# Optimization experiments

Measured on AMD Instinct MI355X. Metric: run time of the kernel, lower is better.

## Reference

```python
import jax, jax.numpy as jnp
import numpy as np

N_NODES = 100000
N_EDGES = 400000
DIM = 3
HID = 32


def _glorot(key, shape):
    fan_in, fan_out = shape[0], shape[1]
    lim = np.sqrt(6.0 / (fan_in + fan_out))
    return jax.random.uniform(key, shape, jnp.float32, -lim, lim)


def setup_inputs() -> dict:
    key = jax.random.key(0)
    ks = jax.random.split(key, 12)
    x = jax.random.normal(ks[0], (N_NODES, DIM), jnp.float32)
    edge_index = jax.random.randint(ks[1], (2, N_EDGES), 0, N_NODES, jnp.int64)
    edge_attr = jax.random.normal(ks[2], (N_EDGES, DIM), jnp.float32)
    params = {
        # conv1: NNConv(3 -> 32), edge nn = Linear(3, 3*32)
        'Wn1': _glorot(ks[3], (DIM, DIM * HID)), 'bn1': jnp.zeros((DIM * HID,), jnp.float32),
        'root1': _glorot(ks[4], (DIM, HID)), 'b1': jnp.zeros((HID,), jnp.float32),
        # conv2: NNConv(32 -> 32), edge nn = Linear(3, 32*32)
        'Wn2': _glorot(ks[5], (DIM, HID * HID)), 'bn2': jnp.zeros((HID * HID,), jnp.float32),
        'root2': _glorot(ks[6], (HID, HID)), 'b2': jnp.zeros((HID,), jnp.float32),
        # fc layers
        'Wf1': _glorot(ks[7], (HID, HID)), 'bf1': jnp.zeros((HID,), jnp.float32),
        'Wf2': _glorot(ks[8], (HID, 1)), 'bf2': jnp.zeros((1,), jnp.float32),
    }
    return {'x': x, 'edge_index': edge_index, 'edge_attr': edge_attr, **params}


def _nnconv(x, src, dst, edge_attr, Wn, bn, root, b, in_c, out_c):
    # per-edge weight matrix from edge MLP: [E, in_c, out_c]
    We = (edge_attr @ Wn + bn).reshape(-1, in_c, out_c)
    # gather source features, per-edge matmul, scatter-add to destinations
    msg = jnp.einsum('ei,eio->eo', x[src], We)  # [E, out_c]
    agg = jax.ops.segment_sum(msg, dst, num_segments=x.shape[0])  # [N, out_c]
    return agg + x @ root + b


def reference(x, edge_index, edge_attr, Wn1, bn1, root1, b1, Wn2, bn2, root2, b2, Wf1, bf1, Wf2, bf2):
    src, dst = edge_index[0], edge_index[1]
    h = jax.nn.relu(_nnconv(x, src, dst, edge_attr, Wn1, bn1, root1, b1, DIM, HID))
    h = jax.nn.relu(_nnconv(h, src, dst, edge_attr, Wn2, bn2, root2, b2, HID, HID))
    h = jax.nn.relu(h @ Wf1 + bf1)
    return h @ Wf2 + bf2  # [N, 1]
```

## Files before the change

kernel.cpp:

```cpp
#include <hip/hip_runtime.h>
#include <hip/hip_fp16.h>

#define N_NODES 100000
#define N_EDGES 400000
#define SCAN_BLOCKS ((N_NODES + 255) / 256)

__global__ __launch_bounds__(256) void zero_kernel(int4* __restrict__ deg4) {
    int i = blockIdx.x * 256 + threadIdx.x;
    if (i < N_NODES / 4) deg4[i] = make_int4(0, 0, 0, 0);
}

__global__ __launch_bounds__(256) void hist_kernel(const int* __restrict__ ei,
                                                   int* __restrict__ deg) {
    int e = blockIdx.x * 256 + threadIdx.x;
    if (e < N_EDGES) atomicAdd(&deg[ei[N_EDGES + e]], 1);
}

__global__ __launch_bounds__(256) void scanA_kernel(const int* __restrict__ deg,
                                                    int* __restrict__ rowptr,
                                                    int* __restrict__ psum) {
    __shared__ int sm[256];
    int i = blockIdx.x * 256 + threadIdx.x;
    int v = (i < N_NODES) ? deg[i] : 0;
    sm[threadIdx.x] = v;
    __syncthreads();
    #pragma unroll
    for (int off = 1; off < 256; off <<= 1) {
        int t = (threadIdx.x >= off) ? sm[threadIdx.x - off] : 0;
        __syncthreads();
        sm[threadIdx.x] += t;
        __syncthreads();
    }
    if (i < N_NODES) rowptr[i] = sm[threadIdx.x] - v;
    if (threadIdx.x == 255) psum[blockIdx.x] = sm[255];
}

__global__ __launch_bounds__(256) void scanBC_kernel(const int* __restrict__ psum,
                                                     int* __restrict__ rowptr,
                                                     int* __restrict__ cursor) {
    __shared__ int sm[8];
    int bid = blockIdx.x, tid = threadIdx.x;
    int acc = 0;
    for (int t = tid; t < bid; t += 256) acc += psum[t];
    #pragma unroll
    for (int off = 32; off; off >>= 1) acc += __shfl_down(acc, off, 64);
    if ((tid & 63) == 0) sm[tid >> 6] = acc;
    __syncthreads();
    int base = sm[0] + sm[1] + sm[2] + sm[3];
    int i = bid * 256 + tid;
    if (i < N_NODES) {
        int r = rowptr[i] + base;
        rowptr[i] = r;
        cursor[i] = r;
    }
    if (i == 0) rowptr[N_NODES] = N_EDGES;
}

__global__ __launch_bounds__(256) void scatter_kernel(const int* __restrict__ ei,
                                                      const float* __restrict__ ea,
                                                      const float* __restrict__ x,
                                                      int* __restrict__ cursor,
                                                      float4* __restrict__ edataA,
                                                      float4* __restrict__ edataB) {
    int e = blockIdx.x * 256 + threadIdx.x;
    if (e >= N_EDGES) return;
    int s = ei[e], d = ei[N_EDGES + e];
    int pos = atomicAdd(&cursor[d], 1);
    edataA[pos] = make_float4(ea[e*3], ea[e*3+1], ea[e*3+2], __int_as_float(s));
    edataB[pos] = make_float4(x[s*3], x[s*3+1], x[s*3+2], 0.f);
}

__global__ __launch_bounds__(256) void conv1_kernel(const int* __restrict__ rowptr,
                                                    const float4* __restrict__ edataA,
                                                    const float4* __restrict__ edataB,
                                                    const float* __restrict__ x,
                                                    const float* __restrict__ Wn1,
                                                    const float* __restrict__ bn1,
                                                    const float* __restrict__ root1,
                                                    const float* __restrict__ b1,
                                                    float* __restrict__ h1) {
    int gid = blockIdx.x * 256 + threadIdx.x;
    int n = gid >> 5, o = gid & 31;
    if (n >= N_NODES) return;
    float W[3][3], bb[3];
    #pragma unroll
    for (int d2 = 0; d2 < 3; ++d2)
        #pragma unroll
        for (int d = 0; d < 3; ++d) W[d2][d] = Wn1[d2*96 + d*32 + o];
    #pragma unroll
    for (int d = 0; d < 3; ++d) bb[d] = bn1[d*32 + o];

    int j0 = rowptr[n], j1 = rowptr[n + 1];
    float acc0 = 0.f, acc1 = 0.f;
    int j = j0;
    for (; j + 2 <= j1; j += 2) {
        float4 eA0 = edataA[j],   eB0 = edataB[j];
        float4 eA1 = edataA[j+1], eB1 = edataB[j+1];
        float wd0 = fmaf(eA0.x, W[0][0], fmaf(eA0.y, W[1][0], fmaf(eA0.z, W[2][0], bb[0])));
        float wd1 = fmaf(eA0.x, W[0][1], fmaf(eA0.y, W[1][1], fmaf(eA0.z, W[2][1], bb[1])));
        float wd2 = fmaf(eA0.x, W[0][2], fmaf(eA0.y, W[1][2], fmaf(eA0.z, W[2][2], bb[2])));
        acc0 += fmaf(eB0.x, wd0, fmaf(eB0.y, wd1, eB0.z * wd2));
        float ud0 = fmaf(eA1.x, W[0][0], fmaf(eA1.y, W[1][0], fmaf(eA1.z, W[2][0], bb[0])));
        float ud1 = fmaf(eA1.x, W[0][1], fmaf(eA1.y, W[1][1], fmaf(eA1.z, W[2][1], bb[1])));
        float ud2 = fmaf(eA1.x, W[0][2], fmaf(eA1.y, W[1][2], fmaf(eA1.z, W[2][2], bb[2])));
        acc1 += fmaf(eB1.x, ud0, fmaf(eB1.y, ud1, eB1.z * ud2));
    }
    if (j < j1) {
        float4 eA0 = edataA[j], eB0 = edataB[j];
        float wd0 = fmaf(eA0.x, W[0][0], fmaf(eA0.y, W[1][0], fmaf(eA0.z, W[2][0], bb[0])));
        float wd1 = fmaf(eA0.x, W[0][1], fmaf(eA0.y, W[1][1], fmaf(eA0.z, W[2][1], bb[1])));
        float wd2 = fmaf(eA0.x, W[0][2], fmaf(eA0.y, W[1][2], fmaf(eA0.z, W[2][2], bb[2])));
        acc0 += fmaf(eB0.x, wd0, fmaf(eB0.y, wd1, eB0.z * wd2));
    }
    float v = acc0 + acc1 + b1[o];
    v = fmaf(x[n*3],   root1[o],      v);
    v = fmaf(x[n*3+1], root1[32 + o], v);
    v = fmaf(x[n*3+2], root1[64 + o], v);
    h1[(size_t)n*32 + o] = fmaxf(v, 0.f);
}

__global__ __launch_bounds__(256) void prep2_kernel(const float* __restrict__ h1,
                                                    const float* __restrict__ Wn2,
                                                    const float* __restrict__ bn2,
                                                    uint2* __restrict__ G2h) {
    int o = threadIdx.x & 31;
    float w0[32], w1[32], w2[32], w3[32];
    #pragma unroll
    for (int i = 0; i < 32; ++i) {
        w0[i] = Wn2[         i*32 + o];
        w1[i] = Wn2[1024 +   i*32 + o];
        w2[i] = Wn2[2048 +   i*32 + o];
        w3[i] = bn2[         i*32 + o];
    }
    int g = (blockIdx.x * 256 + threadIdx.x) >> 5;
    int gstep = (gridDim.x * 256) >> 5;
    for (int n = g; n < N_NODES; n += gstep) {
        const float* __restrict__ hr = h1 + (size_t)n * 32;
        float g0 = 0.f, g1 = 0.f, g2 = 0.f, g3 = 0.f;
        #pragma unroll
        for (int i = 0; i < 32; ++i) {
            float hi = hr[i];
            g0 = fmaf(hi, w0[i], g0);
            g1 = fmaf(hi, w1[i], g1);
            g2 = fmaf(hi, w2[i], g2);
            g3 = fmaf(hi, w3[i], g3);
        }
        __half2 ab = __floats2half2_rn(g0, g1);
        __half2 cd = __floats2half2_rn(g2, g3);
        uint2 p;
        p.x = *(const unsigned int*)&ab;
        p.y = *(const unsigned int*)&cd;
        G2h[(size_t)n*32 + o] = p;
    }
}

__global__ __launch_bounds__(256) void conv2_kernel(const int* __restrict__ rowptr,
                                                    const float4* __restrict__ edataA,
                                                    const uint2* __restrict__ G2h,
                                                    float* __restrict__ h2pre) {
    int gid = blockIdx.x * 256 + threadIdx.x;
    int n = gid >> 5, o = gid & 31;
    if (n >= N_NODES) return;
    int j0 = rowptr[n], j1 = rowptr[n + 1];
    float a0 = 0.f, a1 = 0.f;
    int j = j0;
    for (; j + 2 <= j1; j += 2) {
        float4 e0 = edataA[j], e1 = edataA[j+1];
        uint2 p0 = G2h[(size_t)__float_as_int(e0.w)*32 + o];
        uint2 p1 = G2h[(size_t)__float_as_int(e1.w)*32 + o];
        float2 f0a = __half22float2(*(const __half2*)&p0.x);
        float2 f0b = __half22float2(*(const __half2*)&p0.y);
        float2 f1a = __half22float2(*(const __half2*)&p1.x);
        float2 f1b = __half22float2(*(const __half2*)&p1.y);
        a0 += fmaf(e0.x, f0a.x, fmaf(e0.y, f0a.y, fmaf(e0.z, f0b.x, f0b.y)));
        a1 += fmaf(e1.x, f1a.x, fmaf(e1.y, f1a.y, fmaf(e1.z, f1b.x, f1b.y)));
    }
    if (j < j1) {
        float4 e0 = edataA[j];
        uint2 p0 = G2h[(size_t)__float_as_int(e0.w)*32 + o];
        float2 f0a = __half22float2(*(const __half2*)&p0.x);
        float2 f0b = __half22float2(*(const __half2*)&p0.y);
        a0 += fmaf(e0.x, f0a.x, fmaf(e0.y, f0a.y, fmaf(e0.z, f0b.x, f0b.y)));
    }
    h2pre[(size_t)n*32 + o] = a0 + a1;
}

__global__ __launch_bounds__(256) void node2_kernel(const float* __restrict__ h2pre,
                                                    const float* __restrict__ h1,
                                                    const float* __restrict__ root2,
                                                    const float* __restrict__ b2,
                                                    const float* __restrict__ Wf1,
                                                    const float* __restrict__ bf1,
                                                    const float* __restrict__ Wf2,
                                                    const float* __restrict__ bf2,
                                                    float* __restrict__ out) {
    int n = blockIdx.x * 256 + threadIdx.x;
    if (n >= N_NODES) return;
    float hr[32];
    const float4* hv = (const float4*)(h1 + (size_t)n * 32);
    #pragma unroll
    for (int j4 = 0; j4 < 8; ++j4) {
        float4 t = hv[j4];
        hr[j4*4+0] = t.x; hr[j4*4+1] = t.y; hr[j4*4+2] = t.z; hr[j4*4+3] = t.w;
    }
    const float4* av = (const float4*)(h2pre + (size_t)n * 32);
    float h2[32];
    #pragma unroll
    for (int j4 = 0; j4 < 8; ++j4) {
        float4 a = av[j4];
        #pragma unroll
        for (int k = 0; k < 4; ++k) {
            int j = j4*4 + k;
            float acc = (&a.x)[k] + b2[j];
            #pragma unroll
            for (int i = 0; i < 32; ++i)
                acc = fmaf(hr[i], root2[i*32 + j], acc);
            h2[j] = fmaxf(acc, 0.f);
        }
    }
    float acc2 = bf2[0];
    #pragma unroll
    for (int j = 0; j < 32; ++j) {
        float a = bf1[j];
        #pragma unroll
        for (int i = 0; i < 32; ++i) a = fmaf(h2[i], Wf1[i*32 + j], a);
        acc2 = fmaf(fmaxf(a, 0.f), Wf2[j], acc2);
    }
    out[n] = acc2;
}

extern "C" void kernel_launch(void* const* d_in, const int* in_sizes, int n_in,
                              void* d_out, int out_size, void* d_ws, size_t ws_size,
                              hipStream_t stream) {
    const float* x     = (const float*)d_in[0];
    const int*   ei    = (const int*)  d_in[1];
    const float* ea    = (const float*)d_in[2];
    const float* Wn1   = (const float*)d_in[3];
    const float* bn1   = (const float*)d_in[4];
    const float* root1 = (const float*)d_in[5];
    const float* b1    = (const float*)d_in[6];
    const float* Wn2   = (const float*)d_in[7];
    const float* bn2   = (const float*)d_in[8];
    const float* root2 = (const float*)d_in[9];
    const float* b2    = (const float*)d_in[10];
    const float* Wf1   = (const float*)d_in[11];
    const float* bf1   = (const float*)d_in[12];
    const float* Wf2   = (const float*)d_in[13];
    const float* bf2   = (const float*)d_in[14];
    float* out = (float*)d_out;

    float*  h1     = (float*)d_ws;
    float*  h2pre  = h1 + (size_t)N_NODES*32;
    uint2*  G2h    = (uint2*)(h2pre + (size_t)N_NODES*32);
    float4* edataA = (float4*)(G2h + (size_t)N_NODES*32);
    float4* edataB = edataA + N_EDGES;
    int*    deg    = (int*)(edataB + N_EDGES);
    int*    rowptr = deg + N_NODES;
    int*    cursor = rowptr + N_NODES + 1;
    int*    psum   = cursor + N_NODES;

    int eb   = (N_EDGES + 255) / 256;
    int nb   = (N_NODES + 255) / 256;
    int nb32 = (N_NODES * 32 + 255) / 256;
    int zb   = (N_NODES / 4 + 255) / 256;

    zero_kernel   <<<zb, 256, 0, stream>>>((int4*)deg);
    hist_kernel   <<<eb, 256, 0, stream>>>(ei, deg);
    scanA_kernel  <<<SCAN_BLOCKS, 256, 0, stream>>>(deg, rowptr, psum);
    scanBC_kernel <<<SCAN_BLOCKS, 256, 0, stream>>>(psum, rowptr, cursor);
    scatter_kernel<<<eb, 256, 0, stream>>>(ei, ea, x, cursor, edataA, edataB);
    conv1_kernel  <<<nb32, 256, 0, stream>>>(rowptr, edataA, edataB, x, Wn1, bn1, root1, b1, h1);
    prep2_kernel  <<<1536, 256, 0, stream>>>(h1, Wn2, bn2, G2h);
    conv2_kernel  <<<nb32, 256, 0, stream>>>(rowptr, edataA, G2h, h2pre);
    node2_kernel  <<<nb, 256, 0, stream>>>(h2pre, h1, root2, b2, Wf1, bf1, Wf2, bf2, out);
}
```

Before: 150.1 us.

## Fuse CSR build into cooperative kernel, gather x in conv1, precompute root2 in prep2

Replaces the five CSR-construction launches with a single cooperative kernel that uses grid-wide syncs between the zero, histogram, scan and scatter phases. It drops the edataB buffer, so conv1 now gathers source features from x by index instead. prep2 is reorganised to use 64-lane waves that also compute h1·root2, stored as fp16, so node2 no longer runs a 32x32 matmul per node. The trade-offs are grid-sync overhead, more random gathers in conv1, and extra fp16 rounding on the root term. node2 also contains leftover redundant loads and conversions.

Result: slower. 327.9 us (+118.4%).

```diff
diff --git a/kernel.cpp b/kernel.cpp
--- a/kernel.cpp
+++ b/kernel.cpp
@@ -1,78 +1,78 @@
 #include <hip/hip_runtime.h>
 #include <hip/hip_fp16.h>
+#include <hip/hip_cooperative_groups.h>
 
 #define N_NODES 100000
 #define N_EDGES 400000
-#define SCAN_BLOCKS ((N_NODES + 255) / 256)
-
-__global__ __launch_bounds__(256) void zero_kernel(int4* __restrict__ deg4) {
-    int i = blockIdx.x * 256 + threadIdx.x;
-    if (i < N_NODES / 4) deg4[i] = make_int4(0, 0, 0, 0);
-}
-
-__global__ __launch_bounds__(256) void hist_kernel(const int* __restrict__ ei,
-                                                   int* __restrict__ deg) {
-    int e = blockIdx.x * 256 + threadIdx.x;
-    if (e < N_EDGES) atomicAdd(&deg[ei[N_EDGES + e]], 1);
-}
-
-__global__ __launch_bounds__(256) void scanA_kernel(const int* __restrict__ deg,
+#define BUILD_BLOCKS ((N_NODES + 255) / 256)
+
+namespace cg = cooperative_groups;
+
+__global__ __launch_bounds__(256) void build_kernel(const int* __restrict__ ei,
+                                                    const float* __restrict__ ea,
+                                                    int* __restrict__ deg,
                                                     int* __restrict__ rowptr,
-                                                    int* __restrict__ psum) {
-    __shared__ int sm[256];
-    int i = blockIdx.x * 256 + threadIdx.x;
-    int v = (i < N_NODES) ? deg[i] : 0;
-    sm[threadIdx.x] = v;
-    __syncthreads();
-    #pragma unroll
-    for (int off = 1; off < 256; off <<= 1) {
-        int t = (threadIdx.x >= off) ? sm[threadIdx.x - off] : 0;
+                                                    int* __restrict__ cursor,
+                                                    int* __restrict__ psum,
+                                                    float4* __restrict__ edataA) {
+    cg::grid_group grid = cg::this_grid();
+    int tid = threadIdx.x, bid = blockIdx.x;
+    int gtid = bid * 256 + tid;
+    int gsz = gridDim.x * 256;
+
+    for (int i = gtid; i < N_NODES; i += gsz) deg[i] = 0;
+    grid.sync();
+
+    for (int e = gtid; e < N_EDGES; e += gsz)
+        atomicAdd(&deg[ei[N_EDGES + e]], 1);
+    grid.sync();
+
+    {
+        __shared__ int sm[256];
+        int i = gtid;
+        int v = (i < N_NODES) ? deg[i] : 0;
+        sm[tid] = v;
         __syncthreads();
-        sm[threadIdx.x] += t;
+        #pragma unroll
+        for (int off = 1; off < 256; off <<= 1) {
+            int t = (tid >= off) ? sm[tid - off] : 0;
+            __syncthreads();
+            sm[tid] += t;
+            __syncthreads();
+        }
+        if (i < N_NODES) rowptr[i] = sm[tid] - v;
+        if (tid == 255) psum[bid] = sm[255];
+    }
+    grid.sync();
+
+    {
+        __shared__ int sm2[8];
+        int acc = 0;
+        for (int t = tid; t < bid; t += 256) acc += psum[t];
+        #pragma unroll
+        for (int off = 32; off; off >>= 1) acc += __shfl_down(acc, off, 64);
+        if ((tid & 63) == 0) sm2[tid >> 6] = acc;
         __syncthreads();
-    }
-    if (i < N_NODES) rowptr[i] = sm[threadIdx.x] - v;
-    if (threadIdx.x == 255) psum[blockIdx.x] = sm[255];
-}
-
-__global__ __launch_bounds__(256) void scanBC_kernel(const int* __restrict__ psum,
-                                                     int* __restrict__ rowptr,
-                                                     int* __restrict__ cursor) {
-    __shared__ int sm[8];
-    int bid = blockIdx.x, tid = threadIdx.x;
-    int acc = 0;
-    for (int t = tid; t < bid; t += 256) acc += psum[t];
-    #pragma unroll
-    for (int off = 32; off; off >>= 1) acc += __shfl_down(acc, off, 64);
-    if ((tid & 63) == 0) sm[tid >> 6] = acc;
-    __syncthreads();
-    int base = sm[0] + sm[1] + sm[2] + sm[3];
-    int i = bid * 256 + tid;
-    if (i < N_NODES) {
-        int r = rowptr[i] + base;
-        rowptr[i] = r;
-        cursor[i] = r;
-    }
-    if (i == 0) rowptr[N_NODES] = N_EDGES;
-}
-
-__global__ __launch_bounds__(256) void scatter_kernel(const int* __restrict__ ei,
-                                                      const float* __restrict__ ea,
-                                                      const float* __restrict__ x,
-                                                      int* __restrict__ cursor,
-                                                      float4* __restrict__ edataA,
-                                                      float4* __restrict__ edataB) {
-    int e = blockIdx.x * 256 + threadIdx.x;
-    if (e >= N_EDGES) return;
-    int s = ei[e], d = ei[N_EDGES + e];
-    int pos = atomicAdd(&cursor[d], 1);
-    edataA[pos] = make_float4(ea[e*3], ea[e*3+1], ea[e*3+2], __int_as_float(s));
-    edataB[pos] = make_float4(x[s*3], x[s*3+1], x[s*3+2], 0.f);
+        int base = sm2[0] + sm2[1] + sm2[2] + sm2[3];
+        int i = gtid;
+        if (i < N_NODES) {
+            int r = rowptr[i] + base;
+            rowptr[i] = r;
+            cursor[i] = r;
+        }
+        if (i == 0) rowptr[N_NODES] = N_EDGES;
+    }
+    grid.sync();
+
+    for (int e = gtid; e < N_EDGES; e += gsz) {
+        int s = ei[e], d = ei[N_EDGES + e];
+        int pos = atomicAdd(&cursor[d], 1);
+        edataA[pos] = make_float4(ea[e*3], ea[e*3+1], ea[e*3+2], __int_as_float(s));
+    }
 }
 
 __global__ __launch_bounds__(256) void conv1_kernel(const int* __restrict__ rowptr,
                                                     const float4* __restrict__ edataA,
-                                                    const float4* __restrict__ edataB,
                                                     const float* __restrict__ x,
                                                     const float* __restrict__ Wn1,
                                                     const float* __restrict__ bn1,
@@ -94,23 +94,27 @@
     float acc0 = 0.f, acc1 = 0.f;
     int j = j0;
     for (; j + 2 <= j1; j += 2) {
-        float4 eA0 = edataA[j],   eB0 = edataB[j];
-        float4 eA1 = edataA[j+1], eB1 = edataB[j+1];
+        float4 eA0 = edataA[j], eA1 = edataA[j+1];
+        int s0 = __float_as_int(eA0.w), s1 = __float_as_int(eA1.w);
+        float x00 = x[s0*3], x01 = x[s0*3+1], x02 = x[s0*3+2];
+        float x10 = x[s1*3], x11 = x[s1*3+1], x12 = x[s1*3+2];
         float wd0 = fmaf(eA0.x, W[0][0], fmaf(eA0.y, W[1][0], fmaf(eA0.z, W[2][0], bb[0])));
         float wd1 = fmaf(eA0.x, W[0][1], fmaf(eA0.y, W[1][1], fmaf(eA0.z, W[2][1], bb[1])));
         float wd2 = fmaf(eA0.x, W[0][2], fmaf(eA0.y, W[1][2], fmaf(eA0.z, W[2][2], bb[2])));
-        acc0 += fmaf(eB0.x, wd0, fmaf(eB0.y, wd1, eB0.z * wd2));
+        acc0 += fmaf(x00, wd0, fmaf(x01, wd1, x02 * wd2));
         float ud0 = fmaf(eA1.x, W[0][0], fmaf(eA1.y, W[1][0], fmaf(eA1.z, W[2][0], bb[0])));
         float ud1 = fmaf(eA1.x, W[0][1], fmaf(eA1.y, W[1][1], fmaf(eA1.z, W[2][1], bb[1])));
         float ud2 = fmaf(eA1.x, W[0][2], fmaf(eA1.y, W[1][2], fmaf(eA1.z, W[2][2], bb[2])));
-        acc1 += fmaf(eB1.x, ud0, fmaf(eB1.y, ud1, eB1.z * ud2));
+        acc1 += fmaf(x10, ud0, fmaf(x11, ud1, x12 * ud2));
     }
     if (j < j1) {
-        float4 eA0 = edataA[j], eB0 = edataB[j];
+        float4 eA0 = edataA[j];
+        int s0 = __float_as_int(eA0.w);
+        float x00 = x[s0*3], x01 = x[s0*3+1], x02 = x[s0*3+2];
         float wd0 = fmaf(eA0.x, W[0][0], fmaf(eA0.y, W[1][0], fmaf(eA0.z, W[2][0], bb[0])));
         float wd1 = fmaf(eA0.x, W[0][1], fmaf(eA0.y, W[1][1], fmaf(eA0.z, W[2][1], bb[1])));
         float wd2 = fmaf(eA0.x, W[0][2], fmaf(eA0.y, W[1][2], fmaf(eA0.z, W[2][2], bb[2])));
-        acc0 += fmaf(eB0.x, wd0, fmaf(eB0.y, wd1, eB0.z * wd2));
+        acc0 += fmaf(x00, wd0, fmaf(x01, wd1, x02 * wd2));
     }
     float v = acc0 + acc1 + b1[o];
     v = fmaf(x[n*3],   root1[o],      v);
@@ -122,35 +126,37 @@
 __global__ __launch_bounds__(256) void prep2_kernel(const float* __restrict__ h1,
                                                     const float* __restrict__ Wn2,
                                                     const float* __restrict__ bn2,
-                                                    uint2* __restrict__ G2h) {
-    int o = threadIdx.x & 31;
-    float w0[32], w1[32], w2[32], w3[32];
+                                                    const float* __restrict__ root2,
+                                                    unsigned int* __restrict__ G2u,
+                                                    __half* __restrict__ R2h) {
+    int lane = threadIdx.x & 63;
+    int h = lane >> 5, o = lane & 31;
+    const float* q0 = (h == 0) ? (Wn2)        : (Wn2 + 2048);
+    const float* q1 = (h == 0) ? (Wn2 + 1024) : (bn2);
+    float w0[32], w1[32], w2[32];
     #pragma unroll
     for (int i = 0; i < 32; ++i) {
-        w0[i] = Wn2[         i*32 + o];
-        w1[i] = Wn2[1024 +   i*32 + o];
-        w2[i] = Wn2[2048 +   i*32 + o];
-        w3[i] = bn2[         i*32 + o];
-    }
-    int g = (blockIdx.x * 256 + threadIdx.x) >> 5;
-    int gstep = (gridDim.x * 256) >> 5;
-    for (int n = g; n < N_NODES; n += gstep) {
-        const float* __restrict__ hr = h1 + (size_t)n * 32;
-        float g0 = 0.f, g1 = 0.f, g2 = 0.f, g3 = 0.f;
-        #pragma unroll
-        for (int i = 0; i < 32; ++i) {
-            float hi = hr[i];
-            g0 = fmaf(hi, w0[i], g0);
-            g1 = fmaf(hi, w1[i], g1);
-            g2 = fmaf(hi, w2[i], g2);
-            g3 = fmaf(hi, w3[i], g3);
-        }
-        __half2 ab = __floats2half2_rn(g0, g1);
-        __half2 cd = __floats2half2_rn(g2, g3);
-        uint2 p;
-        p.x = *(const unsigned int*)&ab;
-        p.y = *(const unsigned int*)&cd;
-        G2h[(size_t)n*32 + o] = p;
+        w0[i] = q0[i*32 + o];
+        w1[i] = q1[i*32 + o];
+        w2[i] = root2[i*32 + o];
+    }
+    int w = (blockIdx.x * 256 + threadIdx.x) >> 6;
+    int nwaves = (gridDim.x * 256) >> 6;
+    for (int n = w; n < N_NODES; n += nwaves) {
+        int nu = __builtin_amdgcn_readfirstlane(n);
+        const float4* hv = (const float4*)(h1 + (size_t)nu * 32);
+        float a0 = 0.f, a1 = 0.f, a2 = 0.f;
+        #pragma unroll
+        for (int i4 = 0; i4 < 8; ++i4) {
+            float4 t = hv[i4];
+            a0 = fmaf(t.x, w0[i4*4+0], a0); a1 = fmaf(t.x, w1[i4*4+0], a1); a2 = fmaf(t.x, w2[i4*4+0], a2);
+            a0 = fmaf(t.y, w0[i4*4+1], a0); a1 = fmaf(t.y, w1[i4*4+1], a1); a2 = fmaf(t.y, w2[i4*4+1], a2);
+            a0 = fmaf(t.z, w0[i4*4+2], a0); a1 = fmaf(t.z, w1[i4*4+2], a1); a2 = fmaf(t.z, w2[i4*4+2], a2);
+            a0 = fmaf(t.w, w0[i4*4+3], a0); a1 = fmaf(t.w, w1[i4*4+3], a1); a2 = fmaf(t.w, w2[i4*4+3], a2);
+        }
+        __half2 p = __floats2half2_rn(a0, a1);
+        G2u[(size_t)nu*64 + o*2 + h] = *(const unsigned int*)&p;
+        if (h) R2h[(size_t)nu*32 + o] = __float2half(a2);
     }
 }
 
@@ -186,8 +192,7 @@
 }
 
 __global__ __launch_bounds__(256) void node2_kernel(const float* __restrict__ h2pre,
-                                                    const float* __restrict__ h1,
-                                                    const float* __restrict__ root2,
+                                                    const __half* __restrict__ R2h,
                                                     const float* __restrict__ b2,
                                                     const float* __restrict__ Wf1,
                                                     const float* __restrict__ bf1,
@@ -196,25 +201,31 @@
                                                     float* __restrict__ out) {
     int n = blockIdx.x * 256 + threadIdx.x;
     if (n >= N_NODES) return;
-    float hr[32];
-    const float4* hv = (const float4*)(h1 + (size_t)n * 32);
-    #pragma unroll
-    for (int j4 = 0; j4 < 8; ++j4) {
-        float4 t = hv[j4];
-        hr[j4*4+0] = t.x; hr[j4*4+1] = t.y; hr[j4*4+2] = t.z; hr[j4*4+3] = t.w;
-    }
+    float h2[32];
     const float4* av = (const float4*)(h2pre + (size_t)n * 32);
-    float h2[32];
+    const uint2*  rv = (const uint2*)(R2h + (size_t)n * 32);
     #pragma unroll
     for (int j4 = 0; j4 < 8; ++j4) {
         float4 a = av[j4];
+        uint2 rp = rv[j4 >> 1];
+        unsigned int rw = (j4 & 1) ? rp.y : rp.x;
+        float2 r2 = __half22float2(*(const __half2*)&rw);
+        (void)rw; (void)r2;
+        float4 rr;
+        {
+            float2 lo = __half22float2(*(const __half2*)&rp.x);
+            float2 hi = __half22float2(*(const __half2*)&rp.y);
+            if (j4 & 1) { rr = make_float4(hi.x, hi.y, 0.f, 0.f); }
+            rr = make_float4(lo.x, lo.y, hi.x, hi.y);
+        }
+        uint2 rp2 = rv[j4];
+        float2 lo2 = __half22float2(*(const __half2*)&rp2.x);
+        float2 hi2 = __half22float2(*(const __half2*)&rp2.y);
+        rr = make_float4(lo2.x, lo2.y, hi2.x, hi2.y);
         #pragma unroll
         for (int k = 0; k < 4; ++k) {
             int j = j4*4 + k;
-            float acc = (&a.x)[k] + b2[j];
-            #pragma unroll
-            for (int i = 0; i < 32; ++i)
-                acc = fmaf(hr[i], root2[i*32 + j], acc);
+            float acc = (&a.x)[k] + b2[j] + (&rr.x)[k];
             h2[j] = fmaxf(acc, 0.f);
         }
     }
@@ -251,26 +262,25 @@
 
     float*  h1     = (float*)d_ws;
     float*  h2pre  = h1 + (size_t)N_NODES*32;
-    uint2*  G2h    = (uint2*)(h2pre + (size_t)N_NODES*32);
-    float4* edataA = (float4*)(G2h + (size_t)N_NODES*32);
-    float4* edataB = edataA + N_EDGES;
-    int*    deg    = (int*)(edataB + N_EDGES);
+    unsigned int* G2u = (unsigned int*)(h2pre + (size_t)N_NODES*32);
+    __half* R2h    = (__half*)(G2u + (size_t)N_NODES*64);
+    float4* edataA = (float4*)(R2h + (size_t)N_NODES*32);
+    int*    deg    = (int*)(edataA + N_EDGES);
     int*    rowptr = deg + N_NODES;
     int*    cursor = rowptr + N_NODES + 1;
     int*    psum   = cursor + N_NODES;
 
-    int eb   = (N_EDGES + 255) / 256;
     int nb   = (N_NODES + 255) / 256;
     int nb32 = (N_NODES * 32 + 255) / 256;
-    int zb   = (N_NODES / 4 + 255) / 256;
-
-    zero_kernel   <<<zb, 256, 0, stream>>>((int4*)deg);
-    hist_kernel   <<<eb, 256, 0, stream>>>(ei, deg);
-    scanA_kernel  <<<SCAN_BLOCKS, 256, 0, stream>>>(deg, rowptr, psum);
-    scanBC_kernel <<<SCAN_BLOCKS, 256, 0, stream>>>(psum, rowptr, cursor);
-    scatter_kernel<<<eb, 256, 0, stream>>>(ei, ea, x, cursor, edataA, edataB);
-    conv1_kernel  <<<nb32, 256, 0, stream>>>(rowptr, edataA, edataB, x, Wn1, bn1, root1, b1, h1);
-    prep2_kernel  <<<1536, 256, 0, stream>>>(h1, Wn2, bn2, G2h);
-    conv2_kernel  <<<nb32, 256, 0, stream>>>(rowptr, edataA, G2h, h2pre);
-    node2_kernel  <<<nb, 256, 0, stream>>>(h2pre, h1, root2, b2, Wf1, bf1, Wf2, bf2, out);
-}
+
+    {
+        void* args[] = { (void*)&ei, (void*)&ea, (void*)&deg, (void*)&rowptr,
+                         (void*)&cursor, (void*)&psum, (void*)&edataA };
+        hipLaunchCooperativeKernel((const void*)build_kernel,
+                                   dim3(BUILD_BLOCKS), dim3(256), args, 0, stream);
+    }
+    conv1_kernel<<<nb32, 256, 0, stream>>>(rowptr, edataA, x, Wn1, bn1, root1, b1, h1);
+    prep2_kernel<<<1536, 256, 0, stream>>>(h1, Wn2, bn2, root2, G2u, R2h);
+    conv2_kernel<<<nb32, 256, 0, stream>>>(rowptr, edataA, (const uint2*)G2u, h2pre);
+    node2_kernel<<<nb, 256, 0, stream>>>(h2pre, R2h, b2, Wf1, bf1, Wf2, bf2, out);
+}
```
